# Optimization experiments

Measured on AMD Instinct MI355X. Metric: run time of the kernel, lower is better.

Reference implementation:

```python
import jax, jax.numpy as jnp
import numpy as np
from jax import lax

STRIDE, PAD, K = 1, 1, 3  # module defaults


def setup_inputs() -> dict:
    key = jax.random.key(0)
    k1, k2, k3, k4 = jax.random.split(key, 4)
    N, C, H, W, O = 8, 64, 112, 112, 64
    n = K * K
    x = jax.random.normal(k1, (N, C, H, W), jnp.float32)
    # kaiming-uniform-ish scale for main conv weight
    weight = jax.random.normal(k2, (O, C, K, K), jnp.float32) * (1.0 / np.sqrt(C * K * K))
    bias = jnp.zeros((O,), jnp.float32)
    # small random offset predictor (original zero-inits; small values exercise bilinear path)
    offset_w = jax.random.normal(k3, (3 * n, C, K, K), jnp.float32) * 0.01
    offset_b = jax.random.normal(k4, (3 * n,), jnp.float32) * 0.01
    return {"x": x, "weight": weight, "bias": bias, "offset_w": offset_w, "offset_b": offset_b}


def _bilinear(x, py, px):
    """Zero-padded bilinear sampling. x:[N,C,H,W]; py,px:[N,n,Ho,Wo] -> [N,C,n,Ho,Wo]."""
    N, C, H, W = x.shape
    xf = x.reshape(N, C, H * W)
    y0 = jnp.floor(py)
    x0 = jnp.floor(px)
    out = jnp.zeros((N, C) + py.shape[1:], x.dtype)
    for dy in (0.0, 1.0):
        for dx in (0.0, 1.0):
            yi = y0 + dy
            xi = x0 + dx
            w = (1.0 - jnp.abs(py - yi)) * (1.0 - jnp.abs(px - xi))
            valid = (yi >= 0) & (yi <= H - 1) & (xi >= 0) & (xi <= W - 1)
            yc = jnp.clip(yi, 0, H - 1).astype(jnp.int32)
            xc = jnp.clip(xi, 0, W - 1).astype(jnp.int32)
            idx = (yc * W + xc).reshape(N, 1, -1)
            g = jnp.take_along_axis(xf, jnp.broadcast_to(idx, (N, C, idx.shape[-1])), axis=2)
            g = g.reshape((N, C) + py.shape[1:])
            out = out + g * jnp.where(valid, w, 0.0)[:, None]
    return out


def reference(x, weight, bias, offset_w, offset_b):
    N, C, H, W = x.shape
    O = weight.shape[0]
    n = K * K
    # offset/mask predictor: 3x3 conv -> [N, 3*n, Ho, Wo]
    raw = lax.conv_general_dilated(
        x, offset_w, (STRIDE, STRIDE), [(PAD, PAD), (PAD, PAD)],
        dimension_numbers=("NCHW", "OIHW", "NCHW"),
    ) + offset_b[None, :, None, None]
    Ho, Wo = raw.shape[2], raw.shape[3]
    off = raw[:, : 2 * n].reshape(N, n, 2, Ho, Wo)       # (dy, dx) per tap
    mask = jax.nn.sigmoid(raw[:, 2 * n :])               # [N, n, Ho, Wo]
    # base sampling grid: p0 + kernel tap position
    tap_y = (jnp.arange(n) // K).astype(jnp.float32)[:, None, None]   # [n,1,1]
    tap_x = (jnp.arange(n) % K).astype(jnp.float32)[:, None, None]
    base_y = (jnp.arange(Ho) * STRIDE - PAD).astype(jnp.float32)[None, :, None] + tap_y  # [n,Ho,1]
    base_x = (jnp.arange(Wo) * STRIDE - PAD).astype(jnp.float32)[None, None, :] + tap_x  # [n,1,Wo]
    py = off[:, :, 0] + base_y[None]   # [N,n,Ho,Wo]
    px = off[:, :, 1] + base_x[None]
    sampled = _bilinear(x, py, px)                       # [N,C,n,Ho,Wo]
    val = sampled * mask[:, None]                        # modulation
    out = jnp.einsum("ncthw,oct->nohw", val, weight.reshape(O, C, n))
    return out + bias[None, :, None, None]
```

## Files before the change

kernel.cpp:

```cpp
#include <hip/hip_runtime.h>
#include <hip/hip_fp16.h>
#include <math.h>

#define NB  8
#define CIN 64
#define HH  112
#define WW  112
#define OC  64
#define HWSZ (HH*WW)
#define NPOS (NB*HWSZ)

#define PR 8
#define PC 21
#define NPOSP (PR*PC)
#define PATCH_CHUNKS (NPOSP*8)

#define TP_BLOCKS (HWSZ/64*NB)

typedef unsigned short u16;
typedef __attribute__((ext_vector_type(8))) _Float16 h8;
typedef __attribute__((ext_vector_type(4))) float floatx4;

#define XT_ELEMS   (NB*HWSZ*CIN)
#define WSWZ_ELEMS (18*4*64*8)
#define OSWZ_ELEMS (18*4*32*8)

union CV { uint4 u; h8 h; };

__device__ __forceinline__ u16 f2h(float f) { return __half_as_ushort(__float2half(f)); }
__device__ __forceinline__ __half2 H2(unsigned v) { union { unsigned u; __half2 h; } c; c.u = v; return c.h; }
__device__ __forceinline__ unsigned U2(__half2 h) { union { unsigned u; __half2 h; } c; c.h = h; return c.u; }
__device__ __forceinline__ unsigned pkh(float lo, float hi) {
    union { __half2 h; unsigned u; } c;
    c.h = __floats2half2_rn(lo, hi);
    return c.u;
}

struct TapW { __half2 w00, w01, w10, w11; };

__global__ __launch_bounds__(256) void prep_k(
    const float* __restrict__ x, const float* __restrict__ wgt,
    const float* __restrict__ offw,
    u16* __restrict__ xt, u16* __restrict__ wswz, u16* __restrict__ oswz)
{
    __shared__ float t[64][65];
    const int tid = threadIdx.x;
    const int bid = blockIdx.x;
    if (bid < TP_BLOCKS) {
        const int n   = bid & 7;
        const int hw0 = (bid >> 3) * 64;
        const int wv  = tid & 63;
        const int g   = tid >> 6;
        #pragma unroll
        for (int i = 0; i < 16; ++i) {
            const int c = i*4 + g;
            t[c][wv] = x[((size_t)n*CIN + c)*HWSZ + hw0 + wv];
        }
        __syncthreads();
        #pragma unroll
        for (int i = 0; i < 4; ++i) {
            const int unit = i*256 + tid;
            const int cg = unit & 15;
            const int hw = unit >> 4;
            uint2 o;
            o.x = pkh(t[cg*4+0][hw], t[cg*4+1][hw]);
            o.y = pkh(t[cg*4+2][hw], t[cg*4+3][hw]);
            *(uint2*)(xt + ((size_t)n*HWSZ + hw0 + hw)*CIN + cg*4) = o;
        }
    } else {
        const int gid = (bid - TP_BLOCKS)*256 + tid;
        if (gid < WSWZ_ELEMS) {
            const int j = gid & 7, o = (gid >> 3) & 63, q = (gid >> 9) & 3, s = gid >> 11;
            const int k = s*32 + q*8 + j;
            const int c = k & 63, tt = k >> 6;
            wswz[gid] = f2h(wgt[o*576 + c*9 + tt]);
        } else {
            const int g2 = gid - WSWZ_ELEMS;
            const int j = g2 & 7, r = (g2 >> 3) & 31, q = (g2 >> 8) & 3, s = g2 >> 10;
            const int k = s*32 + q*8 + j;
            const int c = k & 63, tt = k >> 6;
            oswz[g2] = (r < 27) ? f2h(offw[r*576 + c*9 + tt]) : (u16)0;
        }
    }
}

#define IML(DST, S_) { \
    const int t_ = (S_) >> 1; \
    const int ty_ = t_/3, tx_ = t_ - 3*ty_; \
    const int r_ = wid + 1 + ty_; \
    const int c_ = m + 1 + tx_; \
    const int pos_ = r_*PC + c_; \
    const int ck_ = ((S_) & 1)*4 + q; \
    DST = *(const uint4*)(patch + pos_*128 + ((ck_ ^ (pos_ & 7)) << 4)); }

#define OFF_MFMA(SRC, S_) { CV cb_; cb_.u = (SRC); \
    const u16* ap_ = oswz + ((S_)*4 + q)*256 + m*8; \
    acc0 = __builtin_amdgcn_mfma_f32_16x16x32_f16(*(const h8*)(ap_),       cb_.h, acc0, 0, 0, 0); \
    acc1 = __builtin_amdgcn_mfma_f32_16x16x32_f16(*(const h8*)(ap_ + 128), cb_.h, acc1, 0, 0, 0); }

#define HALF_STEP(R00, R01, R10, R11, TW, S_) { \
    CV cb_; \
    cb_.u.x = U2(__hfma2(H2((R00).x),(TW).w00, __hfma2(H2((R01).x),(TW).w01, \
              __hfma2(H2((R10).x),(TW).w10, __hmul2(H2((R11).x),(TW).w11))))); \
    cb_.u.y = U2(__hfma2(H2((R00).y),(TW).w00, __hfma2(H2((R01).y),(TW).w01, \
              __hfma2(H2((R10).y),(TW).w10, __hmul2(H2((R11).y),(TW).w11))))); \
    cb_.u.z = U2(__hfma2(H2((R00).z),(TW).w00, __hfma2(H2((R01).z),(TW).w01, \
              __hfma2(H2((R10).z),(TW).w10, __hmul2(H2((R11).z),(TW).w11))))); \
    cb_.u.w = U2(__hfma2(H2((R00).w),(TW).w00, __hfma2(H2((R01).w),(TW).w01, \
              __hfma2(H2((R10).w),(TW).w10, __hmul2(H2((R11).w),(TW).w11))))); \
    const u16* wp_ = wswz + ((S_)*4 + q)*512 + m*8; \
    acc[0] = __builtin_amdgcn_mfma_f32_16x16x32_f16(*(const h8*)(wp_),       cb_.h, acc[0], 0, 0, 0); \
    acc[1] = __builtin_amdgcn_mfma_f32_16x16x32_f16(*(const h8*)(wp_ + 128), cb_.h, acc[1], 0, 0, 0); \
    acc[2] = __builtin_amdgcn_mfma_f32_16x16x32_f16(*(const h8*)(wp_ + 256), cb_.h, acc[2], 0, 0, 0); \
    acc[3] = __builtin_amdgcn_mfma_f32_16x16x32_f16(*(const h8*)(wp_ + 384), cb_.h, acc[3], 0, 0, 0); }

#define UNPACK_TW(TW, PW) { \
    (TW).w00 = __half2half2(__ushort_as_half((u16)((PW).x & 0xFFFFu))); \
    (TW).w01 = __half2half2(__ushort_as_half((u16)((PW).x >> 16))); \
    (TW).w10 = __half2half2(__ushort_as_half((u16)((PW).y & 0xFFFFu))); \
    (TW).w11 = __half2half2(__ushort_as_half((u16)((PW).y >> 16))); }

__global__ __launch_bounds__(256)
__attribute__((amdgpu_waves_per_eu(5, 8)))
void dcn_k(
    const u16*  __restrict__ xt,
    const u16*  __restrict__ wswz,
    const u16*  __restrict__ oswz,
    const float* __restrict__ bias,
    const float* __restrict__ offb,
    float* __restrict__ out)
{
    __shared__ uint4 patch4[PATCH_CHUNKS];
    __shared__ float rawsm[4][32][16];
    char* patch = (char*)patch4;
    uint2*    prmW = (uint2*)rawsm;
    unsigned* prmO = (unsigned*)((char*)rawsm + 4608);

    const int tid  = threadIdx.x;
    const int lane = tid & 63;
    const int wid  = tid >> 6;
    const int m    = lane & 15;
    const int q    = lane >> 4;

    const int n   = blockIdx.x & 7;
    const int idx = blockIdx.x >> 3;
    const int rg  = idx / 7;
    const int cc  = idx - rg*7;
    const int hoB = rg * 4;
    const int wo0 = cc * 16;
    const int ho  = hoB + wid;
    const u16* xtn = xt + (size_t)n * HWSZ * CIN;

    #pragma unroll
    for (int i = 0; i < 6; ++i) {
        const int u = i*256 + tid;
        if (u < PATCH_CHUNKS) {
            const int pos = u >> 3, ck = u & 7;
            const int pry = pos / PC;
            const int pcx = pos - pry*PC;
            const int gy = hoB - 2 + pry;
            const int gx = wo0 - 2 + pcx;
            uint4 v = {0u,0u,0u,0u};
            if (((unsigned)gy < HH) && ((unsigned)gx < WW))
                v = *(const uint4*)(xtn + (gy*WW + gx)*CIN + ck*8);
            *(uint4*)(patch + pos*128 + ((ck ^ (pos & 7)) << 4)) = v;
        }
    }
    __syncthreads();

    {
        uint4 b[6];
        floatx4 acc0 = {0.f,0.f,0.f,0.f}, acc1 = {0.f,0.f,0.f,0.f};
        #pragma unroll
        for (int s = 0; s < 6; ++s) IML(b[s], s)
        #pragma unroll
        for (int s = 0; s < 6; ++s) {
            uint4 nv; IML(nv, s + 6)
            OFF_MFMA(b[s], s)
            b[s] = nv;
        }
        #pragma unroll
        for (int s = 0; s < 6; ++s) {
            uint4 nv; IML(nv, s + 12)
            OFF_MFMA(b[s], s + 6)
            b[s] = nv;
        }
        #pragma unroll
        for (int s = 0; s < 6; ++s) OFF_MFMA(b[s], s + 12)

        #pragma unroll
        for (int r = 0; r < 4; ++r) {
            rawsm[wid][q*4 + r][m]      = acc0[r];
            rawsm[wid][16 + q*4 + r][m] = acc1[r];
        }
    }
    __syncthreads();

    float vy[3], vx[3], vmk[3];
    #pragma unroll
    for (int i = 0; i < 3; ++i) {
        const int e = i*64 + lane;
        if (e < 144) {
            const int t = e >> 4, p = e & 15;
            vy[i]  = rawsm[wid][2*t][p];
            vx[i]  = rawsm[wid][2*t + 1][p];
            vmk[i] = rawsm[wid][18 + t][p];
        }
    }
    __syncthreads();
    #pragma unroll
    for (int i = 0; i < 3; ++i) {
        const int e = i*64 + lane;
        if (e < 144) {
            const int t = e >> 4;
            const int p = e & 15;
            const int ty = t / 3, tx = t - 3*ty;
            const float py = vy[i] + offb[2*t]     + (float)(ho - 1 + ty);
            const float px = vx[i] + offb[2*t + 1] + (float)(wo0 + p - 1 + tx);
            const float mk = 1.f / (1.f + expf(-(vmk[i] + offb[18 + t])));
            const float y0f = floorf(py), x0f = floorf(px);
            const float fy = py - y0f, fx = px - x0f;
            const int y0 = (int)y0f, x0 = (int)x0f;
            const float gy = 1.f - fy, gx = 1.f - fx;
            const bool vy0 = (unsigned)y0       < HH;
            const bool vy1 = (unsigned)(y0 + 1) < HH;
            const bool vx0 = (unsigned)x0       < WW;
            const bool vx1 = (unsigned)(x0 + 1) < WW;
            const float w00 = (vy0 && vx0) ? gy*gx*mk : 0.f;
            const float w01 = (vy0 && vx1) ? gy*fx*mk : 0.f;
            const float w10 = (vy1 && vx0) ? fy*gx*mk : 0.f;
            const float w11 = (vy1 && vx1) ? fy*fx*mk : 0.f;
            const int yc0 = min(max(y0, 0), HH-1),  yc1 = min(max(y0+1, 0), HH-1);
            const int xc0 = min(max(x0, 0), WW-1),  xc1 = min(max(x0+1, 0), WW-1);
            const unsigned o00 = (unsigned)((yc0*WW + xc0)*CIN);
            const unsigned dxb = (unsigned)(xc1 - xc0);
            const unsigned dyb = (unsigned)(yc1 - yc0);
            const int r0  = yc0 - (hoB - 2);
            const int c0l = xc0 - (wo0 - 2);
            const bool inp = (r0 >= 0) && (r0 + (int)dyb <= PR-1)
                          && (c0l >= 0) && (c0l + (int)dxb <= PC-1);
            const int pos00 = r0*PC + c0l;
            prmO[(wid*9 + t)*16 + p] = o00 | (dxb << 20) | (dyb << 21)
                            | (((unsigned)pos00 & 0xFFu) << 22)
                            | (inp ? (1u << 30) : 0u);
            uint2 Wv;
            Wv.x = (unsigned)__half_as_ushort(__float2half(w00))
                 | ((unsigned)__half_as_ushort(__float2half(w01)) << 16);
            Wv.y = (unsigned)__half_as_ushort(__float2half(w10))
                 | ((unsigned)__half_as_ushort(__float2half(w11)) << 16);
            prmW[(wid*9 + t)*16 + p] = Wv;
        }
    }
    __syncthreads();

    floatx4 acc[4];
    #pragma unroll
    for (int i = 0; i < 4; ++i) acc[i] = (floatx4){0.f,0.f,0.f,0.f};

    const unsigned* PoB = prmO + wid*9*16 + m;
    const uint2*    PwB = prmW + wid*9*16 + m;

    unsigned band = 0xFFFFFFFFu;
    #pragma unroll
    for (int t = 0; t < 9; ++t) band &= PoB[t*16];

    if (__all((int)((band >> 30) & 1u))) {
        unsigned Po = PoB[0];
        uint2    Pw = PwB[0];
        #pragma unroll
        for (int t = 0; t < 9; ++t) {
            const unsigned PoN = (t < 8) ? PoB[(t+1)*16] : 0u;
            const uint2    PwN = (t < 8) ? PwB[(t+1)*16] : Pw;
            const int p00 = (int)((Po >> 22) & 0xFFu);
            const int dxb = (int)((Po >> 20) & 1u);
            const int dyb = (int)((Po >> 21) & 1u);
            const int p01 = p00 + dxb;
            const int p10 = p00 + dyb*PC;
            const int p11 = p10 + dxb;
            const int a00 = p00*128 + ((q ^ (p00 & 7)) << 4);
            const int a01 = p01*128 + ((q ^ (p01 & 7)) << 4);
            const int a10 = p10*128 + ((q ^ (p10 & 7)) << 4);
            const int a11 = p11*128 + ((q ^ (p11 & 7)) << 4);
            const uint4 g0 = *(const uint4*)(patch + a00);
            const uint4 g1 = *(const uint4*)(patch + a01);
            const uint4 g2 = *(const uint4*)(patch + a10);
            const uint4 g3 = *(const uint4*)(patch + a11);
            const uint4 g4 = *(const uint4*)(patch + (a00 ^ 64));
            const uint4 g5 = *(const uint4*)(patch + (a01 ^ 64));
            const uint4 g6 = *(const uint4*)(patch + (a10 ^ 64));
            const uint4 g7 = *(const uint4*)(patch + (a11 ^ 64));
            TapW tw; UNPACK_TW(tw, Pw)
            HALF_STEP(g0, g1, g2, g3, tw, 2*t)
            HALF_STEP(g4, g5, g6, g7, tw, 2*t + 1)
            Po = PoN; Pw = PwN;
        }
    } else {
        const int ch0 = q*8, ch1 = 32 + q*8;
        #pragma unroll
        for (int t = 0; t < 9; ++t) {
            const unsigned Po = PoB[t*16];
            const uint2    Pw = PwB[t*16];
            TapW tw; UNPACK_TW(tw, Pw)
            uint4 g0,g1,g2,g3,g4,g5,g6,g7;
            if (__all((int)((Po >> 30) & 1u))) {
                const int p00 = (int)((Po >> 22) & 0xFFu);
                const int dxb = (int)((Po >> 20) & 1u);
                const int dyb = (int)((Po >> 21) & 1u);
                const int p01 = p00 + dxb;
                const int p10 = p00 + dyb*PC;
                const int p11 = p10 + dxb;
                const int a00 = p00*128 + ((q ^ (p00 & 7)) << 4);
                const int a01 = p01*128 + ((q ^ (p01 & 7)) << 4);
                const int a10 = p10*128 + ((q ^ (p10 & 7)) << 4);
                const int a11 = p11*128 + ((q ^ (p11 & 7)) << 4);
                g0 = *(const uint4*)(patch + a00);
                g1 = *(const uint4*)(patch + a01);
                g2 = *(const uint4*)(patch + a10);
                g3 = *(const uint4*)(patch + a11);
                g4 = *(const uint4*)(patch + (a00 ^ 64));
                g5 = *(const uint4*)(patch + (a01 ^ 64));
                g6 = *(const uint4*)(patch + (a10 ^ 64));
                g7 = *(const uint4*)(patch + (a11 ^ 64));
            } else {
                const int o00 = (int)(Po & 0xFFFFFu);
                const int dx  = (int)((Po >> 20) & 1u) << 6;
                const int dy  = (int)((Po >> 21) & 1u) * (WW*CIN);
                g0 = *(const uint4*)(xtn + o00 + ch0);
                g1 = *(const uint4*)(xtn + o00 + dx + ch0);
                g2 = *(const uint4*)(xtn + o00 + dy + ch0);
                g3 = *(const uint4*)(xtn + o00 + dx + dy + ch0);
                g4 = *(const uint4*)(xtn + o00 + ch1);
                g5 = *(const uint4*)(xtn + o00 + dx + ch1);
                g6 = *(const uint4*)(xtn + o00 + dy + ch1);
                g7 = *(const uint4*)(xtn + o00 + dx + dy + ch1);
            }
            HALF_STEP(g0, g1, g2, g3, tw, 2*t)
            HALF_STEP(g4, g5, g6, g7, tw, 2*t + 1)
        }
    }

    #pragma unroll
    for (int ob = 0; ob < 4; ++ob) {
        #pragma unroll
        for (int r = 0; r < 4; ++r) {
            const int o = ob*16 + q*4 + r;
            out[(((size_t)n*OC + o)*HH + ho)*WW + wo0 + m] = acc[ob][r] + bias[o];
        }
    }
}

extern "C" void kernel_launch(void* const* d_in, const int* in_sizes, int n_in,
                              void* d_out, int out_size, void* d_ws, size_t ws_size,
                              hipStream_t stream)
{
    const float* x    = (const float*)d_in[0];
    const float* wgt  = (const float*)d_in[1];
    const float* bias = (const float*)d_in[2];
    const float* offw = (const float*)d_in[3];
    const float* offb = (const float*)d_in[4];
    float* out = (float*)d_out;

    u16* xt   = (u16*)d_ws;
    u16* wswz = xt + XT_ELEMS;
    u16* oswz = wswz + WSWZ_ELEMS;

    prep_k<<<dim3(TP_BLOCKS + (WSWZ_ELEMS + OSWZ_ELEMS)/256), 256, 0, stream>>>(
        x, wgt, offw, xt, wswz, oswz);
    dcn_k<<<dim3(NPOS/64), 256, 0, stream>>>(xt, wswz, oswz, bias, offb, out);
}
```

Baseline: 114.8 us.

## Load patch via direct-to-LDS and overlap it with offset conv from global

Interior blocks now fill the shared-memory input patch with global_load_lds, which copies global memory straight into LDS and skips the register round-trip. Border blocks keep the old zero-padded path. The offset-predictor im2col operands are now read from global memory instead of the patch, so the barrier after the patch fill is removed and the patch load overlaps the offset MFMAs. Per-tap sampling parameters are also packed into one uint4 per entry so each tap needs a single LDS read. The trade-off is more global/L1 traffic for the offset conv, and it relies on the later barrier to make the async LDS writes visible.

New measurement: 131.1 us. +14.2%, slower.

```diff
diff --git a/kernel.cpp b/kernel.cpp
--- a/kernel.cpp
+++ b/kernel.cpp
@@ -37,6 +37,12 @@
 }
 
 struct TapW { __half2 w00, w01, w10, w11; };
+
+__device__ __forceinline__ void gload_lds16(const u16* gsrc, void* ldst) {
+    __builtin_amdgcn_global_load_lds(
+        (const __attribute__((address_space(1))) unsigned*)gsrc,
+        (__attribute__((address_space(3))) unsigned*)ldst, 16, 0, 0);
+}
 
 __global__ __launch_bounds__(256) void prep_k(
     const float* __restrict__ x, const float* __restrict__ wgt,
@@ -84,14 +90,15 @@
     }
 }
 
-#define IML(DST, S_) { \
+#define IM2COL_LOAD(DST, S_) { \
     const int t_ = (S_) >> 1; \
     const int ty_ = t_/3, tx_ = t_ - 3*ty_; \
-    const int r_ = wid + 1 + ty_; \
-    const int c_ = m + 1 + tx_; \
-    const int pos_ = r_*PC + c_; \
-    const int ck_ = ((S_) & 1)*4 + q; \
-    DST = *(const uint4*)(patch + pos_*128 + ((ck_ ^ (pos_ & 7)) << 4)); }
+    const int y_ = ho - 1 + ty_, xx_ = wo0 + m - 1 + tx_; \
+    const int ch_ = ((S_) & 1)*32 + q*8; \
+    uint4 v_ = {0u,0u,0u,0u}; \
+    if (((unsigned)y_ < HH) && ((unsigned)xx_ < WW)) \
+        v_ = *(const uint4*)(xtn + (y_*WW + xx_)*CIN + ch_); \
+    DST = v_; }
 
 #define OFF_MFMA(SRC, S_) { CV cb_; cb_.u = (SRC); \
     const u16* ap_ = oswz + ((S_)*4 + q)*256 + m*8; \
@@ -114,11 +121,11 @@
     acc[2] = __builtin_amdgcn_mfma_f32_16x16x32_f16(*(const h8*)(wp_ + 256), cb_.h, acc[2], 0, 0, 0); \
     acc[3] = __builtin_amdgcn_mfma_f32_16x16x32_f16(*(const h8*)(wp_ + 384), cb_.h, acc[3], 0, 0, 0); }
 
-#define UNPACK_TW(TW, PW) { \
-    (TW).w00 = __half2half2(__ushort_as_half((u16)((PW).x & 0xFFFFu))); \
-    (TW).w01 = __half2half2(__ushort_as_half((u16)((PW).x >> 16))); \
-    (TW).w10 = __half2half2(__ushort_as_half((u16)((PW).y & 0xFFFFu))); \
-    (TW).w11 = __half2half2(__ushort_as_half((u16)((PW).y >> 16))); }
+#define UNPACK_TW(TW, WX, WY) { \
+    (TW).w00 = __half2half2(__ushort_as_half((u16)((WX) & 0xFFFFu))); \
+    (TW).w01 = __half2half2(__ushort_as_half((u16)((WX) >> 16))); \
+    (TW).w10 = __half2half2(__ushort_as_half((u16)((WY) & 0xFFFFu))); \
+    (TW).w11 = __half2half2(__ushort_as_half((u16)((WY) >> 16))); }
 
 __global__ __launch_bounds__(256)
 __attribute__((amdgpu_waves_per_eu(5, 8)))
@@ -131,10 +138,10 @@
     float* __restrict__ out)
 {
     __shared__ uint4 patch4[PATCH_CHUNKS];
-    __shared__ float rawsm[4][32][16];
-    char* patch = (char*)patch4;
-    uint2*    prmW = (uint2*)rawsm;
-    unsigned* prmO = (unsigned*)((char*)rawsm + 4608);
+    __shared__ uint4 shx4[576];
+    char*  patch = (char*)patch4;
+    float* rawf  = (float*)shx4;
+    uint4* prmQ  = shx4;
 
     const int tid  = threadIdx.x;
     const int lane = tid & 63;
@@ -151,47 +158,63 @@
     const int ho  = hoB + wid;
     const u16* xtn = xt + (size_t)n * HWSZ * CIN;
 
-    #pragma unroll
-    for (int i = 0; i < 6; ++i) {
-        const int u = i*256 + tid;
-        if (u < PATCH_CHUNKS) {
-            const int pos = u >> 3, ck = u & 7;
-            const int pry = pos / PC;
-            const int pcx = pos - pry*PC;
-            const int gy = hoB - 2 + pry;
-            const int gx = wo0 - 2 + pcx;
-            uint4 v = {0u,0u,0u,0u};
-            if (((unsigned)gy < HH) && ((unsigned)gx < WW))
-                v = *(const uint4*)(xtn + (gy*WW + gx)*CIN + ck*8);
-            *(uint4*)(patch + pos*128 + ((ck ^ (pos & 7)) << 4)) = v;
-        }
-    }
-    __syncthreads();
+    const bool interior = (rg >= 1) && (rg <= 26) && (cc >= 1) && (cc <= 5);
+    if (interior) {
+        #pragma unroll
+        for (int i = 0; i < 6; ++i) {
+            const int j = wid + i*4;
+            if (j < 21) {
+                const int s   = j*64 + lane;
+                const int pos = s >> 3;
+                const int ck  = (s & 7) ^ (pos & 7);
+                const int pry = pos / PC;
+                const int pcx = pos - pry*PC;
+                const int gy  = hoB - 2 + pry;
+                const int gx  = wo0 - 2 + pcx;
+                gload_lds16(xtn + (gy*WW + gx)*CIN + ck*8, patch + j*1024);
+            }
+        }
+    } else {
+        #pragma unroll
+        for (int i = 0; i < 6; ++i) {
+            const int u = i*256 + tid;
+            if (u < PATCH_CHUNKS) {
+                const int pos = u >> 3, ck = u & 7;
+                const int pry = pos / PC;
+                const int pcx = pos - pry*PC;
+                const int gy = hoB - 2 + pry;
+                const int gx = wo0 - 2 + pcx;
+                uint4 v = {0u,0u,0u,0u};
+                if (((unsigned)gy < HH) && ((unsigned)gx < WW))
+                    v = *(const uint4*)(xtn + (gy*WW + gx)*CIN + ck*8);
+                *(uint4*)(patch + pos*128 + ((ck ^ (pos & 7)) << 4)) = v;
+            }
+        }
+    }
 
     {
-        uint4 b[6];
+        uint4 buA[6], buB[6];
+        #pragma unroll
+        for (int s = 0; s < 6; ++s) IM2COL_LOAD(buA[s], s)
+        #pragma unroll
+        for (int s = 0; s < 6; ++s) IM2COL_LOAD(buB[s], s + 6)
+
         floatx4 acc0 = {0.f,0.f,0.f,0.f}, acc1 = {0.f,0.f,0.f,0.f};
         #pragma unroll
-        for (int s = 0; s < 6; ++s) IML(b[s], s)
-        #pragma unroll
         for (int s = 0; s < 6; ++s) {
-            uint4 nv; IML(nv, s + 6)
-            OFF_MFMA(b[s], s)
-            b[s] = nv;
-        }
-        #pragma unroll
-        for (int s = 0; s < 6; ++s) {
-            uint4 nv; IML(nv, s + 12)
-            OFF_MFMA(b[s], s + 6)
-            b[s] = nv;
-        }
-        #pragma unroll
-        for (int s = 0; s < 6; ++s) OFF_MFMA(b[s], s + 12)
+            uint4 nv; IM2COL_LOAD(nv, s + 12)
+            OFF_MFMA(buA[s], s)
+            buA[s] = nv;
+        }
+        #pragma unroll
+        for (int s = 0; s < 6; ++s) OFF_MFMA(buB[s], s + 6)
+        #pragma unroll
+        for (int s = 0; s < 6; ++s) OFF_MFMA(buA[s], s + 12)
 
         #pragma unroll
         for (int r = 0; r < 4; ++r) {
-            rawsm[wid][q*4 + r][m]      = acc0[r];
-            rawsm[wid][16 + q*4 + r][m] = acc1[r];
+            rawf[(wid*32 + q*4 + r)*16 + m]      = acc0[r];
+            rawf[(wid*32 + 16 + q*4 + r)*16 + m] = acc1[r];
         }
     }
     __syncthreads();
@@ -202,9 +225,9 @@
         const int e = i*64 + lane;
         if (e < 144) {
             const int t = e >> 4, p = e & 15;
-            vy[i]  = rawsm[wid][2*t][p];
-            vx[i]  = rawsm[wid][2*t + 1][p];
-            vmk[i] = rawsm[wid][18 + t][p];
+            vy[i]  = rawf[(wid*32 + 2*t)*16 + p];
+            vx[i]  = rawf[(wid*32 + 2*t + 1)*16 + p];
+            vmk[i] = rawf[(wid*32 + 18 + t)*16 + p];
         }
     }
     __syncthreads();
@@ -240,15 +263,16 @@
             const bool inp = (r0 >= 0) && (r0 + (int)dyb <= PR-1)
                           && (c0l >= 0) && (c0l + (int)dxb <= PC-1);
             const int pos00 = r0*PC + c0l;
-            prmO[(wid*9 + t)*16 + p] = o00 | (dxb << 20) | (dyb << 21)
-                            | (((unsigned)pos00 & 0xFFu) << 22)
-                            | (inp ? (1u << 30) : 0u);
-            uint2 Wv;
-            Wv.x = (unsigned)__half_as_ushort(__float2half(w00))
-                 | ((unsigned)__half_as_ushort(__float2half(w01)) << 16);
-            Wv.y = (unsigned)__half_as_ushort(__float2half(w10))
-                 | ((unsigned)__half_as_ushort(__float2half(w11)) << 16);
-            prmW[(wid*9 + t)*16 + p] = Wv;
+            uint4 P;
+            P.x = o00 | (dxb << 20) | (dyb << 21)
+                | (((unsigned)pos00 & 0xFFu) << 22)
+                | (inp ? (1u << 30) : 0u);
+            P.y = (unsigned)__half_as_ushort(__float2half(w00))
+                | ((unsigned)__half_as_ushort(__float2half(w01)) << 16);
+            P.z = (unsigned)__half_as_ushort(__float2half(w10))
+                | ((unsigned)__half_as_ushort(__float2half(w11)) << 16);
+            P.w = 0u;
+            prmQ[wid*144 + e] = P;
         }
     }
     __syncthreads();
@@ -257,23 +281,21 @@
     #pragma unroll
     for (int i = 0; i < 4; ++i) acc[i] = (floatx4){0.f,0.f,0.f,0.f};
 
-    const unsigned* PoB = prmO + wid*9*16 + m;
-    const uint2*    PwB = prmW + wid*9*16 + m;
+    const uint4*    PB  = prmQ + wid*144 + m;
+    const unsigned* PBw = (const unsigned*)PB;
 
     unsigned band = 0xFFFFFFFFu;
     #pragma unroll
-    for (int t = 0; t < 9; ++t) band &= PoB[t*16];
+    for (int t = 0; t < 9; ++t) band &= PBw[t*64];
 
     if (__all((int)((band >> 30) & 1u))) {
-        unsigned Po = PoB[0];
-        uint2    Pw = PwB[0];
+        uint4 P = PB[0];
         #pragma unroll
         for (int t = 0; t < 9; ++t) {
-            const unsigned PoN = (t < 8) ? PoB[(t+1)*16] : 0u;
-            const uint2    PwN = (t < 8) ? PwB[(t+1)*16] : Pw;
-            const int p00 = (int)((Po >> 22) & 0xFFu);
-            const int dxb = (int)((Po >> 20) & 1u);
-            const int dyb = (int)((Po >> 21) & 1u);
+            const uint4 PN = (t < 8) ? PB[(t+1)*16] : P;
+            const int p00 = (int)((P.x >> 22) & 0xFFu);
+            const int dxb = (int)((P.x >> 20) & 1u);
+            const int dyb = (int)((P.x >> 21) & 1u);
             const int p01 = p00 + dxb;
             const int p10 = p00 + dyb*PC;
             const int p11 = p10 + dxb;
@@ -289,23 +311,22 @@
             const uint4 g5 = *(const uint4*)(patch + (a01 ^ 64));
             const uint4 g6 = *(const uint4*)(patch + (a10 ^ 64));
             const uint4 g7 = *(const uint4*)(patch + (a11 ^ 64));
-            TapW tw; UNPACK_TW(tw, Pw)
+            TapW tw; UNPACK_TW(tw, P.y, P.z)
             HALF_STEP(g0, g1, g2, g3, tw, 2*t)
             HALF_STEP(g4, g5, g6, g7, tw, 2*t + 1)
-            Po = PoN; Pw = PwN;
+            P = PN;
         }
     } else {
         const int ch0 = q*8, ch1 = 32 + q*8;
         #pragma unroll
         for (int t = 0; t < 9; ++t) {
-            const unsigned Po = PoB[t*16];
-            const uint2    Pw = PwB[t*16];
-            TapW tw; UNPACK_TW(tw, Pw)
+            const uint4 P = PB[t*16];
+            TapW tw; UNPACK_TW(tw, P.y, P.z)
             uint4 g0,g1,g2,g3,g4,g5,g6,g7;
-            if (__all((int)((Po >> 30) & 1u))) {
-                const int p00 = (int)((Po >> 22) & 0xFFu);
-                const int dxb = (int)((Po >> 20) & 1u);
-                const int dyb = (int)((Po >> 21) & 1u);
+            if (__all((int)((P.x >> 30) & 1u))) {
+                const int p00 = (int)((P.x >> 22) & 0xFFu);
+                const int dxb = (int)((P.x >> 20) & 1u);
+                const int dyb = (int)((P.x >> 21) & 1u);
                 const int p01 = p00 + dxb;
                 const int p10 = p00 + dyb*PC;
                 const int p11 = p10 + dxb;
@@ -322,9 +343,9 @@
                 g6 = *(const uint4*)(patch + (a10 ^ 64));
                 g7 = *(const uint4*)(patch + (a11 ^ 64));
             } else {
-                const int o00 = (int)(Po & 0xFFFFFu);
-                const int dx  = (int)((Po >> 20) & 1u) << 6;
-                const int dy  = (int)((Po >> 21) & 1u) * (WW*CIN);
+                const int o00 = (int)(P.x & 0xFFFFFu);
+                const int dx  = (int)((P.x >> 20) & 1u) << 6;
+                const int dy  = (int)((P.x >> 21) & 1u) * (WW*CIN);
                 g0 = *(const uint4*)(xtn + o00 + ch0);
                 g1 = *(const uint4*)(xtn + o00 + dx + ch0);
                 g2 = *(const uint4*)(xtn + o00 + dy + ch0);
```
